# Performance work log

Measured on AMD Instinct MI355X. Metric: run time of the kernel, lower is better.

## Reference

```python
import jax, jax.numpy as jnp
import numpy as np

B, C, H, W = 32, 3, 257, 257
MASK, STRIDE = 17, 4
N = (H - MASK) // STRIDE + 1  # 61 windows per spatial axis
NUM_EDGES = 65                # 64 quantization bins
G_MEAN, G_STD = 0.5, 0.25     # global_mean / global_std init args


def setup_inputs() -> dict:
    key = jax.random.key(0)
    kx, = jax.random.split(key, 1)
    x = jax.random.uniform(kx, (B, C, H, W), dtype=jnp.float32)
    bins = jnp.linspace(0.0, 1.0, NUM_EDGES, dtype=jnp.float32)  # sorted edges
    return {"x": x, "bins": bins}


def _windows(x):
    # Overlapping strided windows, same layout as np.lib.stride_tricks.as_strided:
    # (B, C, N, N, MASK, MASK)
    idx = (jnp.arange(N) * STRIDE)[:, None] + jnp.arange(MASK)[None, :]  # (N, MASK)
    return x[:, :, idx[:, None, :, None], idx[None, :, None, :]]


def reference(x, bins):
    sw = _windows(x)  # (B, C, 61, 61, 17, 17)
    means = sw.mean(axis=(-2, -1))
    std = sw.std(axis=(-2, -1))      # population std (ddof=0), matches numpy default
    maxs = sw.max(axis=(-2, -1))
    mins = sw.min(axis=(-2, -1))
    # NOTE: faithful to source, which uses `maximums` (not means) in the first stat
    s = jnp.concatenate(
        [(maxs - G_MEAN) / G_STD,
         std / G_STD,
         (maxs - means) / G_STD,
         (means - mins) / G_STD],
        axis=1,
    )  # (B, 4C, 61, 61)
    # Quantizer: flatten last two dims, digitize, -1, reshape back
    q = (jnp.digitize(sw.reshape(B, C, N, N, -1), bins) - 1).reshape(sw.shape)
    return sw, s, q
```

## Files before the change

kernel.cpp:

```cpp
#include <hip/hip_runtime.h>

#define BB 32
#define CC 3
#define HH 257
#define WW 257
#define MASK 17
#define STRIDE 4
#define NWIN 61

constexpr int WIN_ELEMS = MASK * MASK;
constexpr int ROW_ELEMS = NWIN * WIN_ELEMS;
constexpr int LDSP = 260;
constexpr long long SW_SIZE = (long long)BB * CC * NWIN * NWIN * WIN_ELEMS;
constexpr long long S_SIZE  = (long long)BB * 4 * CC * NWIN * NWIN;
constexpr int NN2 = NWIN * NWIN;

static __device__ __forceinline__ void compute_elem(
        const float* __restrict__ lds, int o, float& sv, float& qv) {
    int j = o / WIN_ELEMS;
    int r = o - j * WIN_ELEMS;
    int u = r / MASK;
    int v = r - u * MASK;
    float xv = lds[u * LDSP + j * STRIDE + v];
    int qi = (int)floorf(xv * 64.0f);
    qi = qi < -1 ? -1 : (qi > 64 ? 64 : qi);
    sv = xv;
    qv = (float)qi;
}

__global__ __launch_bounds__(256) void leafnet_kernel(
        const float* __restrict__ x,
        float* __restrict__ sw_out,
        float* __restrict__ s_out,
        float* __restrict__ q_out) {
    __shared__ float lds[MASK * LDSP];

    const int bid = blockIdx.x;
    const int i = bid % NWIN;
    const int c = (bid / NWIN) % CC;
    const int b = bid / (NWIN * CC);
    const int tid = threadIdx.x;

    const float* xbase = x + ((size_t)(b * CC + c) * HH + (size_t)i * STRIDE) * WW;
    for (int e = tid; e < MASK * WW; e += 256) {
        int u = e / WW;
        int w = e - u * WW;
        lds[u * LDSP + w] = xbase[e];
    }
    __syncthreads();

    const size_t obase = (size_t)bid * ROW_ELEMS;
    const size_t gend  = obase + ROW_ELEMS;
    const size_t g0    = (obase + 3) & ~(size_t)3;
    const size_t gbe   = gend & ~(size_t)3;
    const int head  = (int)(g0 - obase);
    const int tailn = (int)(gend - gbe);
    const int body  = (int)((gbe - g0) >> 2);

    if (tid < 8) {
        int o = -1;
        if (tid < head) o = tid;
        else if (tid - head < tailn) o = (int)(gbe - obase) + (tid - head);
        if (o >= 0) {
            float sv, qv;
            compute_elem(lds, o, sv, qv);
            sw_out[obase + o] = sv;
            q_out[obase + o] = qv;
        }
    }

    for (int k = tid; k < body; k += 256) {
        size_t g = g0 + ((size_t)k << 2);
        int o = (int)(g - obase);
        float s0, s1, s2, s3, q0, q1, q2, q3;
        compute_elem(lds, o + 0, s0, q0);
        compute_elem(lds, o + 1, s1, q1);
        compute_elem(lds, o + 2, s2, q2);
        compute_elem(lds, o + 3, s3, q3);
        *reinterpret_cast<float4*>(sw_out + g) = make_float4(s0, s1, s2, s3);
        *reinterpret_cast<float4*>(q_out + g)  = make_float4(q0, q1, q2, q3);
    }

    const int lane = tid & 63;
    const int wave = tid >> 6;
    const int j = (lane >> 2) + (wave << 4);
    const int q = lane & 3;

    float sum = 0.0f, sumsq = 0.0f, mx = -1e30f, mn = 1e30f;
    if (j < NWIN) {
        const int e0 = 72 * q;
        const int lim = (q == 3) ? 73 : 72;
        const int jbase = j * STRIDE;
        for (int s = 0; s < lim; ++s) {
            int e = e0 + s;
            int u = e / MASK;
            int v = e - u * MASK;
            float xv = lds[u * LDSP + jbase + v];
            sum += xv;
            sumsq += xv * xv;
            mx = fmaxf(mx, xv);
            mn = fminf(mn, xv);
        }
    }
    sum   += __shfl_xor(sum, 1, 64);
    sumsq += __shfl_xor(sumsq, 1, 64);
    mx = fmaxf(mx, __shfl_xor(mx, 1, 64));
    mn = fminf(mn, __shfl_xor(mn, 1, 64));
    sum   += __shfl_xor(sum, 2, 64);
    sumsq += __shfl_xor(sumsq, 2, 64);
    mx = fmaxf(mx, __shfl_xor(mx, 2, 64));
    mn = fminf(mn, __shfl_xor(mn, 2, 64));

    if (q == 0 && j < NWIN) {
        const float inv_n = 1.0f / (float)WIN_ELEMS;
        float mean = sum * inv_n;
        float var = fmaxf(sumsq * inv_n - mean * mean, 0.0f);
        float sd = sqrtf(var);
        const float inv_std = 4.0f;
        size_t sb = (size_t)b * 12 * NN2 + (size_t)c * NN2 + (size_t)i * NWIN + j;
        s_out[sb + 0 * (size_t)CC * NN2] = (mx - 0.5f) * inv_std;
        s_out[sb + 1 * (size_t)CC * NN2] = sd * inv_std;
        s_out[sb + 2 * (size_t)CC * NN2] = (mx - mean) * inv_std;
        s_out[sb + 3 * (size_t)CC * NN2] = (mean - mn) * inv_std;
    }
}

extern "C" void kernel_launch(void* const* d_in, const int* in_sizes, int n_in,
                              void* d_out, int out_size, void* d_ws, size_t ws_size,
                              hipStream_t stream) {
    const float* x = (const float*)d_in[0];
    float* out = (float*)d_out;
    float* sw_out = out;
    float* s_out  = out + SW_SIZE;
    float* q_out  = out + SW_SIZE + S_SIZE;

    const int grid = BB * CC * NWIN;
    leafnet_kernel<<<grid, 256, 0, stream>>>(x, sw_out, s_out, q_out);
}
```

Before: 949.1 us.

## Use nontemporal stores, swizzle LDS indices, remap block order, shift variance accumulation

Output stores for sw, q and s now use nontemporal stores so the large write stream bypasses cache retention. LDS addresses are XOR-swizzled to reduce bank conflicts on the strided window reads. Block IDs are permuted so that consecutive hardware blocks are spread across eight chunks of the logical grid, which may change how work lands on XCDs. Mean and variance accumulation is shifted by 0.5 for better numerical stability, at the cost of one extra subtract per element.

Measured after the change: 890.4 us. -6.2%, faster.

```diff
diff --git a/kernel.cpp b/kernel.cpp
--- a/kernel.cpp
+++ b/kernel.cpp
@@ -14,6 +14,19 @@
 constexpr long long SW_SIZE = (long long)BB * CC * NWIN * NWIN * WIN_ELEMS;
 constexpr long long S_SIZE  = (long long)BB * 4 * CC * NWIN * NWIN;
 constexpr int NN2 = NWIN * NWIN;
+constexpr int NBLK = BB * CC * NWIN;
+
+typedef float vf4 __attribute__((ext_vector_type(4)));
+
+#if defined(__has_builtin) && __has_builtin(__builtin_nontemporal_store)
+#define NT_STORE(v, p) __builtin_nontemporal_store((v), (p))
+#else
+#define NT_STORE(v, p) (*(p) = (v))
+#endif
+
+static __device__ __forceinline__ int swz(int w) {
+    return w ^ ((w >> 5) & 3);
+}
 
 static __device__ __forceinline__ void compute_elem(
         const float* __restrict__ lds, int o, float& sv, float& qv) {
@@ -21,7 +34,7 @@
     int r = o - j * WIN_ELEMS;
     int u = r / MASK;
     int v = r - u * MASK;
-    float xv = lds[u * LDSP + j * STRIDE + v];
+    float xv = lds[swz(u * LDSP + j * STRIDE + v)];
     int qi = (int)floorf(xv * 64.0f);
     qi = qi < -1 ? -1 : (qi > 64 ? 64 : qi);
     sv = xv;
@@ -35,7 +48,8 @@
         float* __restrict__ q_out) {
     __shared__ float lds[MASK * LDSP];
 
-    const int bid = blockIdx.x;
+    const int hw = blockIdx.x;
+    const int bid = (hw & 7) * (NBLK / 8) + (hw >> 3);
     const int i = bid % NWIN;
     const int c = (bid / NWIN) % CC;
     const int b = bid / (NWIN * CC);
@@ -45,7 +59,7 @@
     for (int e = tid; e < MASK * WW; e += 256) {
         int u = e / WW;
         int w = e - u * WW;
-        lds[u * LDSP + w] = xbase[e];
+        lds[swz(u * LDSP + w)] = xbase[e];
     }
     __syncthreads();
 
@@ -64,8 +78,8 @@
         if (o >= 0) {
             float sv, qv;
             compute_elem(lds, o, sv, qv);
-            sw_out[obase + o] = sv;
-            q_out[obase + o] = qv;
+            NT_STORE(sv, sw_out + obase + o);
+            NT_STORE(qv, q_out + obase + o);
         }
     }
 
@@ -77,8 +91,10 @@
         compute_elem(lds, o + 1, s1, q1);
         compute_elem(lds, o + 2, s2, q2);
         compute_elem(lds, o + 3, s3, q3);
-        *reinterpret_cast<float4*>(sw_out + g) = make_float4(s0, s1, s2, s3);
-        *reinterpret_cast<float4*>(q_out + g)  = make_float4(q0, q1, q2, q3);
+        vf4 sv = {s0, s1, s2, s3};
+        vf4 qv = {q0, q1, q2, q3};
+        NT_STORE(sv, reinterpret_cast<vf4*>(sw_out + g));
+        NT_STORE(qv, reinterpret_cast<vf4*>(q_out + g));
     }
 
     const int lane = tid & 63;
@@ -95,9 +111,10 @@
             int e = e0 + s;
             int u = e / MASK;
             int v = e - u * MASK;
-            float xv = lds[u * LDSP + jbase + v];
-            sum += xv;
-            sumsq += xv * xv;
+            float xv = lds[swz(u * LDSP + jbase + v)];
+            float xs = xv - 0.5f;
+            sum += xs;
+            sumsq += xs * xs;
             mx = fmaxf(mx, xv);
             mn = fminf(mn, xv);
         }
@@ -113,15 +130,16 @@
 
     if (q == 0 && j < NWIN) {
         const float inv_n = 1.0f / (float)WIN_ELEMS;
-        float mean = sum * inv_n;
-        float var = fmaxf(sumsq * inv_n - mean * mean, 0.0f);
+        float ms = sum * inv_n;
+        float mean = 0.5f + ms;
+        float var = fmaxf(sumsq * inv_n - ms * ms, 0.0f);
         float sd = sqrtf(var);
         const float inv_std = 4.0f;
         size_t sb = (size_t)b * 12 * NN2 + (size_t)c * NN2 + (size_t)i * NWIN + j;
-        s_out[sb + 0 * (size_t)CC * NN2] = (mx - 0.5f) * inv_std;
-        s_out[sb + 1 * (size_t)CC * NN2] = sd * inv_std;
-        s_out[sb + 2 * (size_t)CC * NN2] = (mx - mean) * inv_std;
-        s_out[sb + 3 * (size_t)CC * NN2] = (mean - mn) * inv_std;
+        NT_STORE((mx - 0.5f) * inv_std, s_out + sb + 0 * (size_t)CC * NN2);
+        NT_STORE(sd * inv_std,          s_out + sb + 1 * (size_t)CC * NN2);
+        NT_STORE((mx - mean) * inv_std, s_out + sb + 2 * (size_t)CC * NN2);
+        NT_STORE((mean - mn) * inv_std, s_out + sb + 3 * (size_t)CC * NN2);
     }
 }
 
@@ -134,6 +152,5 @@
     float* s_out  = out + SW_SIZE;
     float* q_out  = out + SW_SIZE + S_SIZE;
 
-    const int grid = BB * CC * NWIN;
-    leafnet_kernel<<<grid, 256, 0, stream>>>(x, sw_out, s_out, q_out);
+    leafnet_kernel<<<NBLK, 256, 0, stream>>>(x, sw_out, s_out, q_out);
 }
```
